# Kernel tuning notes

Measured on AMD Instinct MI355X. Metric: run time of the kernel, lower is better.

## Reference

```python
import jax, jax.numpy as jnp
import numpy as np

N_ATOM, N_QUERY, KNN = 100000, 20000, 32
E = N_QUERY * KNN
HID, EDGE_F, HEADS = 128, 16, 8
D_HEAD = HID // HEADS
LN_EPS = 1e-5


def setup_inputs() -> dict:
    key = jax.random.key(0)
    ks = jax.random.split(key, 16)
    s = 1.0 / np.sqrt(HID)
    src = jax.random.randint(ks[0], (E,), 0, N_ATOM)
    dst = jnp.repeat(jnp.arange(N_QUERY), KNN)  # each query has KNN incoming edges
    return {
        "h_atom": jax.random.normal(ks[1], (N_ATOM, HID), jnp.float32),
        "h_query": jax.random.normal(ks[2], (N_QUERY, HID), jnp.float32),
        "edge_attr": jax.random.uniform(ks[3], (E, EDGE_F), jnp.float32),
        "W_q": jax.random.normal(ks[4], (HID, HID), jnp.float32) * s,
        "W_k": jax.random.normal(ks[5], (HID, HID), jnp.float32) * s,
        "W_v": jax.random.normal(ks[6], (HID, HID), jnp.float32) * s,
        "W_rbf": jax.random.normal(ks[7], (HEADS, EDGE_F), jnp.float32) * (1.0 / np.sqrt(EDGE_F)),
        "W1": jax.random.normal(ks[8], (HID, 2 * HID), jnp.float32) * (1.0 / np.sqrt(2 * HID)),
        "b1": jnp.zeros((HID,), jnp.float32),
        "W2": jax.random.normal(ks[9], (HID, HID), jnp.float32) * s,
        "b2": jnp.zeros((HID,), jnp.float32),
        "ln_gamma": jnp.ones((HID,), jnp.float32),
        "ln_beta": jnp.zeros((HID,), jnp.float32),
        "edge_index": jnp.stack([src, dst]),
        "n_query": N_QUERY,
    }


def reference(h_atom, h_query, edge_attr, W_q, W_k, W_v, W_rbf, W1, b1, W2, b2,
              ln_gamma, ln_beta, edge_index, n_query):
    src, dst = edge_index[0], edge_index[1]
    En = src.shape[0]
    # gather + project, per-edge multi-head Q/K/V  [E, H, d]
    Q = (h_query[dst] @ W_q.T).reshape(En, HEADS, D_HEAD)
    K = (h_atom[src] @ W_k.T).reshape(En, HEADS, D_HEAD)
    V = (h_atom[src] @ W_v.T).reshape(En, HEADS, D_HEAD)
    scores = jnp.einsum("ehd,ehd->eh", Q, K) / np.sqrt(D_HEAD) + edge_attr @ W_rbf.T  # [E,H]
    # segment softmax over edges sharing the same dst query, per head
    seg_max = jax.lax.stop_gradient(jax.ops.segment_max(scores, dst, num_segments=n_query))
    ex = jnp.exp(scores - seg_max[dst])
    denom = jax.ops.segment_sum(ex, dst, num_segments=n_query)
    alpha = ex / (denom[dst] + 1e-16)  # [E,H]
    # weighted scatter-add aggregation
    msgs = (alpha[:, :, None] * V).reshape(En, HID)
    agg = jax.ops.segment_sum(msgs, dst, num_segments=n_query)  # [Nq, HID]
    # update MLP + residual + LayerNorm
    z = jnp.concatenate([h_query, agg], axis=-1)
    delta = jax.nn.relu(z @ W1.T + b1) @ W2.T + b2
    y = h_query + delta
    mu = y.mean(-1, keepdims=True)
    var = y.var(-1, keepdims=True)
    return (y - mu) / jnp.sqrt(var + LN_EPS) * ln_gamma + ln_beta
```

## Files before the change

### kernel.cpp

```cpp
#include <hip/hip_runtime.h>
#include <hip/hip_bf16.h>
#include <math.h>

#define N_ATOM   100000
#define N_QUERY  20000
#define KNN      32

typedef __attribute__((ext_vector_type(8))) short  short8;
typedef __attribute__((ext_vector_type(4))) float  floatx4;
typedef __attribute__((ext_vector_type(2))) float  fx2;

static __device__ __forceinline__ unsigned short f2bf_bits(float f) {
  union { __hip_bfloat16 h; unsigned short u; } cv;
  cv.h = __float2bfloat16(f);
  return cv.u;
}
static __device__ __forceinline__ float bflo(unsigned int u) { return __uint_as_float(u << 16); }
static __device__ __forceinline__ float bfhi(unsigned int u) { return __uint_as_float(u & 0xffff0000u); }

__global__ void pack_all_kernel(const float* __restrict__ Wq, const float* __restrict__ Wk,
                                const float* __restrict__ Wv, const float* __restrict__ W1,
                                const float* __restrict__ W2,
                                unsigned short* __restrict__ WKVp, unsigned short* __restrict__ WQp,
                                unsigned short* __restrict__ W1p,  unsigned short* __restrict__ W2p) {
  int tid = blockIdx.x * blockDim.x + threadIdx.x;
  if (tid >= 98304) return;
  const float *Wa, *Wb; int nsplit, Kd, Nd; unsigned short* dst; float scale = 1.0f;
  int t = tid;
  if (t < 32768)      { Wa = Wk; Wb = Wv; nsplit = 128; Kd = 128; Nd = 256; dst = WKVp; }
  else if (t < 49152) { t -= 32768; Wa = Wq; Wb = Wq; nsplit = 128; Kd = 128; Nd = 128; dst = WQp; scale = 0.25f; }
  else if (t < 81920) { t -= 49152; Wa = W1; Wb = W1; nsplit = 128; Kd = 256; Nd = 128; dst = W1p; }
  else                { t -= 81920; Wa = W2; Wb = W2; nsplit = 128; Kd = 128; Nd = 128; dst = W2p; }
  int j    = t & 7;
  int lane = (t >> 3) & 63;
  int t2   = t >> 9;
  int NT   = Nd >> 4;
  int ntile = t2 % NT;
  int ktile = t2 / NT;
  int k = ktile * 32 + (lane >> 4) * 8 + j;
  int n = ntile * 16 + (lane & 15);
  float v = (n < nsplit) ? Wa[(size_t)n * Kd + k] : Wb[(size_t)(n - nsplit) * Kd + k];
  dst[t] = f2bf_bits(v * scale);
}

__global__ __launch_bounds__(256) void gemm_kvq(
    const float* __restrict__ h_atom, const float* __restrict__ h_query,
    const unsigned short* __restrict__ WKVp, const unsigned short* __restrict__ WQp,
    unsigned char* __restrict__ Kp8, unsigned char* __restrict__ Vp8,
    unsigned short* __restrict__ Qb) {
  constexpr int KB = (N_ATOM + 63) / 64;
  __shared__ char lds[16384];
  const int l    = threadIdx.x & 63;
  const int w    = threadIdx.x >> 6;
  const int quad = l >> 4;
  const int col0 = l & 15;

  if ((int)blockIdx.x < KB) {
    const int row0 = blockIdx.x * 64 + w * 16;
    int arow = row0 + col0;
    if (arow >= N_ATOM) arow = N_ATOM - 1;

    const float* aptr = h_atom + (size_t)arow * 128 + quad * 8;
    floatx4 a[8];
#pragma unroll
    for (int k0 = 0; k0 < 4; k0++) {
      a[2 * k0]     = *(const floatx4*)(aptr + k0 * 32);
      a[2 * k0 + 1] = *(const floatx4*)(aptr + k0 * 32 + 4);
    }
    short8 af[4];
#pragma unroll
    for (int k0 = 0; k0 < 4; k0++) {
      af[k0][0] = (short)f2bf_bits(a[2*k0][0]); af[k0][1] = (short)f2bf_bits(a[2*k0][1]);
      af[k0][2] = (short)f2bf_bits(a[2*k0][2]); af[k0][3] = (short)f2bf_bits(a[2*k0][3]);
      af[k0][4] = (short)f2bf_bits(a[2*k0+1][0]); af[k0][5] = (short)f2bf_bits(a[2*k0+1][1]);
      af[k0][6] = (short)f2bf_bits(a[2*k0+1][2]); af[k0][7] = (short)f2bf_bits(a[2*k0+1][3]);
    }

    floatx4 acc[16];
#pragma unroll
    for (int i = 0; i < 16; i++) acc[i] = (floatx4){0.f, 0.f, 0.f, 0.f};
#pragma unroll
    for (int k0 = 0; k0 < 4; k0++) {
      const unsigned short* bbase = WKVp + (size_t)k0 * 16 * 512 + l * 8;
#pragma unroll
      for (int nt = 0; nt < 16; nt++) {
        short8 bf = *(const short8*)(bbase + nt * 512);
        acc[nt] = __builtin_amdgcn_mfma_f32_16x16x32_bf16(af[k0], bf, acc[nt], 0, 0, 0);
      }
    }
#pragma unroll
    for (int nt = 0; nt < 16; nt++) {
#pragma unroll
      for (int r = 0; r < 4; r++) {
        int rl = w * 16 + quad * 4 + r;
        int c  = nt * 16 + col0;
        int pk = __builtin_amdgcn_cvt_pk_fp8_f32(acc[nt][r], acc[nt][r], 0, false);
        if (c < 128) lds[rl * 128 + c] = (char)(pk & 0xff);
        else         lds[8192 + rl * 128 + (c - 128)] = (char)(pk & 0xff);
      }
    }
    __syncthreads();
    const int row0g = blockIdx.x * 64;
#pragma unroll
    for (int it = 0; it < 2; it++) {
      int off = threadIdx.x * 16 + it * 4096;
      if (row0g + (off >> 7) < N_ATOM)
        *(float4*)(Kp8 + (size_t)row0g * 128 + off) = *(const float4*)&lds[off];
    }
#pragma unroll
    for (int it = 0; it < 2; it++) {
      int off = threadIdx.x * 16 + it * 4096;
      if (row0g + (off >> 7) < N_ATOM)
        *(float4*)(Vp8 + (size_t)row0g * 128 + off) = *(const float4*)&lds[8192 + off];
    }
  } else {
    const int row0 = ((int)blockIdx.x - KB) * 64 + w * 16;
    int arow = row0 + col0;
    if (arow >= N_QUERY) arow = N_QUERY - 1;
    floatx4 acc[8];
#pragma unroll
    for (int i = 0; i < 8; i++) acc[i] = (floatx4){0.f, 0.f, 0.f, 0.f};
    const float* aptr = h_query + (size_t)arow * 128 + quad * 8;
#pragma unroll
    for (int k0 = 0; k0 < 128; k0 += 32) {
      floatx4 a0 = *(const floatx4*)(aptr + k0);
      floatx4 a1 = *(const floatx4*)(aptr + k0 + 4);
      short8 af;
      af[0] = (short)f2bf_bits(a0[0]); af[1] = (short)f2bf_bits(a0[1]);
      af[2] = (short)f2bf_bits(a0[2]); af[3] = (short)f2bf_bits(a0[3]);
      af[4] = (short)f2bf_bits(a1[0]); af[5] = (short)f2bf_bits(a1[1]);
      af[6] = (short)f2bf_bits(a1[2]); af[7] = (short)f2bf_bits(a1[3]);
      const unsigned short* bbase = WQp + (size_t)(k0 >> 5) * 8 * 512 + l * 8;
#pragma unroll
      for (int nt = 0; nt < 8; nt++) {
        short8 bf = *(const short8*)(bbase + nt * 512);
        acc[nt] = __builtin_amdgcn_mfma_f32_16x16x32_bf16(af, bf, acc[nt], 0, 0, 0);
      }
    }
#pragma unroll
    for (int nt = 0; nt < 8; nt++) {
#pragma unroll
      for (int r = 0; r < 4; r++) {
        int row = row0 + quad * 4 + r;
        if (row < N_QUERY) Qb[(size_t)row * 128 + nt * 16 + col0] = f2bf_bits(acc[nt][r]);
      }
    }
  }
}

__global__ __launch_bounds__(256) void attn_kernel(
    const unsigned short* __restrict__ Qb,
    const unsigned char* __restrict__ Kp8,
    const unsigned char* __restrict__ Vp8,
    const float* __restrict__ edge_attr,
    const float* __restrict__ Wrbf,
    const int* __restrict__ src,
    float* __restrict__ Agg) {
  const int l = threadIdx.x & 63;
  const int w = threadIdx.x >> 6;
  const int q = blockIdx.x * 4 + w;
  const int j = l >> 3;
  const int h = l & 7;

  const int e0 = q * KNN;
  int srcj = (l < KNN) ? src[e0 + l] : 0;

  float qd[16];
  {
    const unsigned int* qp = (const unsigned int*)(Qb + (size_t)q * 128 + h * 16);
#pragma unroll
    for (int i = 0; i < 8; i++) {
      unsigned int u = qp[i];
      qd[2 * i] = bflo(u); qd[2 * i + 1] = bfhi(u);
    }
  }
  float wr[16];
  {
    const float* wp = Wrbf + h * 16;
#pragma unroll
    for (int i = 0; i < 16; i++) wr[i] = wp[i];
  }

  float acc[16];
#pragma unroll
  for (int i = 0; i < 16; i++) acc[i] = 0.f;
  float lsum = 0.f;

#pragma unroll
  for (int p = 0; p < 4; p++) {
    const int e = p * 8 + j;
    int s = __shfl(srcj, e, 64);
    uint4 kq = *(const uint4*)(Kp8 + (size_t)s * 128 + h * 16);
    uint4 vq = *(const uint4*)(Vp8 + (size_t)s * 128 + h * 16);
    const float4* ep = (const float4*)(edge_attr + (size_t)(e0 + e) * 16);
    float4 ea0 = ep[0], ea1 = ep[1], ea2 = ep[2], ea3 = ep[3];

    float kd = 0.f;
    {
      fx2 f0, f1;
      f0 = __builtin_amdgcn_cvt_pk_f32_fp8((int)kq.x, false);
      f1 = __builtin_amdgcn_cvt_pk_f32_fp8((int)kq.x, true);
      kd += qd[0] * f0[0] + qd[1] * f0[1] + qd[2] * f1[0] + qd[3] * f1[1];
      f0 = __builtin_amdgcn_cvt_pk_f32_fp8((int)kq.y, false);
      f1 = __builtin_amdgcn_cvt_pk_f32_fp8((int)kq.y, true);
      kd += qd[4] * f0[0] + qd[5] * f0[1] + qd[6] * f1[0] + qd[7] * f1[1];
      f0 = __builtin_amdgcn_cvt_pk_f32_fp8((int)kq.z, false);
      f1 = __builtin_amdgcn_cvt_pk_f32_fp8((int)kq.z, true);
      kd += qd[8] * f0[0] + qd[9] * f0[1] + qd[10] * f1[0] + qd[11] * f1[1];
      f0 = __builtin_amdgcn_cvt_pk_f32_fp8((int)kq.w, false);
      f1 = __builtin_amdgcn_cvt_pk_f32_fp8((int)kq.w, true);
      kd += qd[12] * f0[0] + qd[13] * f0[1] + qd[14] * f1[0] + qd[15] * f1[1];
    }
    float ed = wr[0]*ea0.x + wr[1]*ea0.y + wr[2]*ea0.z + wr[3]*ea0.w
             + wr[4]*ea1.x + wr[5]*ea1.y + wr[6]*ea1.z + wr[7]*ea1.w
             + wr[8]*ea2.x + wr[9]*ea2.y + wr[10]*ea2.z + wr[11]*ea2.w
             + wr[12]*ea3.x + wr[13]*ea3.y + wr[14]*ea3.z + wr[15]*ea3.w;

    float pe = __expf(kd + ed);
    lsum += pe;
    {
      fx2 g0, g1;
      g0 = __builtin_amdgcn_cvt_pk_f32_fp8((int)vq.x, false);
      g1 = __builtin_amdgcn_cvt_pk_f32_fp8((int)vq.x, true);
      acc[0] += pe * g0[0]; acc[1] += pe * g0[1]; acc[2] += pe * g1[0]; acc[3] += pe * g1[1];
      g0 = __builtin_amdgcn_cvt_pk_f32_fp8((int)vq.y, false);
      g1 = __builtin_amdgcn_cvt_pk_f32_fp8((int)vq.y, true);
      acc[4] += pe * g0[0]; acc[5] += pe * g0[1]; acc[6] += pe * g1[0]; acc[7] += pe * g1[1];
      g0 = __builtin_amdgcn_cvt_pk_f32_fp8((int)vq.z, false);
      g1 = __builtin_amdgcn_cvt_pk_f32_fp8((int)vq.z, true);
      acc[8] += pe * g0[0]; acc[9] += pe * g0[1]; acc[10] += pe * g1[0]; acc[11] += pe * g1[1];
      g0 = __builtin_amdgcn_cvt_pk_f32_fp8((int)vq.w, false);
      g1 = __builtin_amdgcn_cvt_pk_f32_fp8((int)vq.w, true);
      acc[12] += pe * g0[0]; acc[13] += pe * g0[1]; acc[14] += pe * g1[0]; acc[15] += pe * g1[1];
    }
  }

#pragma unroll
  for (int mask = 8; mask <= 32; mask <<= 1) {
    lsum += __shfl_xor(lsum, mask, 64);
#pragma unroll
    for (int i = 0; i < 16; i++) acc[i] += __shfl_xor(acc[i], mask, 64);
  }
  float inv = 1.f / (lsum + 1e-16f);
  float* dst = Agg + (size_t)q * 128 + h * 16;
  if (j == 0) {
    float4 o0 = {acc[0] * inv, acc[1] * inv, acc[2] * inv, acc[3] * inv};
    float4 o1 = {acc[4] * inv, acc[5] * inv, acc[6] * inv, acc[7] * inv};
    *(float4*)(dst)     = o0;
    *(float4*)(dst + 4) = o1;
  } else if (j == 1) {
    float4 o2 = {acc[8] * inv, acc[9] * inv, acc[10] * inv, acc[11] * inv};
    float4 o3 = {acc[12] * inv, acc[13] * inv, acc[14] * inv, acc[15] * inv};
    *(float4*)(dst + 8)  = o2;
    *(float4*)(dst + 12) = o3;
  }
}

__global__ __launch_bounds__(256) void mlp_kernel(
    const float* __restrict__ h_query, const float* __restrict__ Agg,
    const unsigned short* __restrict__ W1p, const unsigned short* __restrict__ W2p,
    const float* __restrict__ b1, const float* __restrict__ b2,
    const float* __restrict__ gamma, const float* __restrict__ beta,
    float* __restrict__ out) {
  constexpr int M = N_QUERY;
  constexpr int STRIDE = 136;
  __shared__ unsigned short hid[64 * STRIDE];

  const int l    = threadIdx.x & 63;
  const int w    = threadIdx.x >> 6;
  const int quad = l >> 4;
  const int col0 = l & 15;
  const int row0 = blockIdx.x * 64 + w * 16;
  int arow = row0 + col0;
  if (arow >= M) arow = M - 1;

  floatx4 acc[8];
#pragma unroll
  for (int i = 0; i < 8; i++) acc[i] = (floatx4){0.f, 0.f, 0.f, 0.f};
#pragma unroll
  for (int k0 = 0; k0 < 256; k0 += 32) {
    const float* sp = (k0 < 128) ? (h_query + (size_t)arow * 128 + k0)
                                 : (Agg + (size_t)arow * 128 + (k0 - 128));
    floatx4 a0 = *(const floatx4*)(sp + quad * 8);
    floatx4 a1 = *(const floatx4*)(sp + quad * 8 + 4);
    short8 af;
    af[0] = (short)f2bf_bits(a0[0]); af[1] = (short)f2bf_bits(a0[1]);
    af[2] = (short)f2bf_bits(a0[2]); af[3] = (short)f2bf_bits(a0[3]);
    af[4] = (short)f2bf_bits(a1[0]); af[5] = (short)f2bf_bits(a1[1]);
    af[6] = (short)f2bf_bits(a1[2]); af[7] = (short)f2bf_bits(a1[3]);
    const unsigned short* bbase = W1p + (size_t)(k0 >> 5) * 8 * 512 + l * 8;
#pragma unroll
    for (int nt = 0; nt < 8; nt++) {
      short8 bf = *(const short8*)(bbase + nt * 512);
      acc[nt] = __builtin_amdgcn_mfma_f32_16x16x32_bf16(af, bf, acc[nt], 0, 0, 0);
    }
  }
#pragma unroll
  for (int nt = 0; nt < 8; nt++) {
#pragma unroll
    for (int r = 0; r < 4; r++) {
      int rl = w * 16 + quad * 4 + r;
      float v = acc[nt][r] + b1[nt * 16 + col0];
      hid[rl * STRIDE + nt * 16 + col0] = f2bf_bits(fmaxf(v, 0.f));
    }
  }
  __syncthreads();

  floatx4 acc2[8];
#pragma unroll
  for (int i = 0; i < 8; i++) acc2[i] = (floatx4){0.f, 0.f, 0.f, 0.f};
  const int rloc = w * 16 + col0;
#pragma unroll
  for (int k0 = 0; k0 < 128; k0 += 32) {
    short8 af = *(const short8*)(hid + rloc * STRIDE + k0 + quad * 8);
    const unsigned short* bbase = W2p + (size_t)(k0 >> 5) * 8 * 512 + l * 8;
#pragma unroll
    for (int nt = 0; nt < 8; nt++) {
      short8 bf = *(const short8*)(bbase + nt * 512);
      acc2[nt] = __builtin_amdgcn_mfma_f32_16x16x32_bf16(af, bf, acc2[nt], 0, 0, 0);
    }
  }

#pragma unroll
  for (int r = 0; r < 4; r++) {
    int row = row0 + quad * 4 + r;
    int rr  = row < M ? row : M - 1;
    float v[8];
    float s1 = 0.f, s2 = 0.f;
#pragma unroll
    for (int nt = 0; nt < 8; nt++) {
      int c = nt * 16 + col0;
      v[nt] = acc2[nt][r] + b2[c] + h_query[(size_t)rr * 128 + c];
      s1 += v[nt];
    }
    s1 += __shfl_xor(s1, 1, 64); s1 += __shfl_xor(s1, 2, 64);
    s1 += __shfl_xor(s1, 4, 64); s1 += __shfl_xor(s1, 8, 64);
#pragma unroll
    for (int nt = 0; nt < 8; nt++) s2 += v[nt] * v[nt];
    s2 += __shfl_xor(s2, 1, 64); s2 += __shfl_xor(s2, 2, 64);
    s2 += __shfl_xor(s2, 4, 64); s2 += __shfl_xor(s2, 8, 64);
    float mean = s1 * (1.0f / 128.0f);
    float var  = s2 * (1.0f / 128.0f) - mean * mean;
    float rstd = rsqrtf(var + 1e-5f);
    if (row < M) {
#pragma unroll
      for (int nt = 0; nt < 8; nt++) {
        int c = nt * 16 + col0;
        out[(size_t)row * 128 + c] = (v[nt] - mean) * rstd * gamma[c] + beta[c];
      }
    }
  }
}

extern "C" void kernel_launch(void* const* d_in, const int* in_sizes, int n_in,
                              void* d_out, int out_size, void* d_ws, size_t ws_size,
                              hipStream_t stream) {
  const float* h_atom    = (const float*)d_in[0];
  const float* h_query   = (const float*)d_in[1];
  const float* edge_attr = (const float*)d_in[2];
  const float* W_q  = (const float*)d_in[3];
  const float* W_k  = (const float*)d_in[4];
  const float* W_v  = (const float*)d_in[5];
  const float* Wrbf = (const float*)d_in[6];
  const float* W1   = (const float*)d_in[7];
  const float* b1   = (const float*)d_in[8];
  const float* W2   = (const float*)d_in[9];
  const float* b2   = (const float*)d_in[10];
  const float* ln_g = (const float*)d_in[11];
  const float* ln_b = (const float*)d_in[12];
  const int* edge_index = (const int*)d_in[13];
  float* out = (float*)d_out;

  char* ws = (char*)d_ws;
  unsigned char*  Kp8 = (unsigned char*)(ws);
  unsigned char*  Vp8 = (unsigned char*)(ws + 12800000);
  unsigned short* Qb  = (unsigned short*)(ws + 25600000);
  float* Agg          = (float*)(ws + 30720000);
  unsigned short* WKVp = (unsigned short*)(ws + 40960000);
  unsigned short* WQp  = WKVp + 32768;
  unsigned short* W1p  = WQp  + 16384;
  unsigned short* W2p  = W1p  + 32768;

  pack_all_kernel<<<(98304 + 255) / 256, 256, 0, stream>>>(
      W_q, W_k, W_v, W1, W2, WKVp, WQp, W1p, W2p);

  constexpr int KB = (N_ATOM + 63) / 64;
  constexpr int QB = (N_QUERY + 63) / 64;
  gemm_kvq<<<KB + QB, 256, 0, stream>>>(h_atom, h_query, WKVp, WQp, Kp8, Vp8, Qb);

  attn_kernel<<<N_QUERY / 4, 256, 0, stream>>>(Qb, Kp8, Vp8, edge_attr, Wrbf, edge_index, Agg);

  mlp_kernel<<<(N_QUERY + 63) / 64, 256, 0, stream>>>(
      h_query, Agg, W1p, W2p, b1, b2, ln_g, ln_b, out);
}
```

Baseline: 220.1 us.

## Transpose MFMA operands for vector stores, hoist attention loads, use split-reduce

Swaps the A/B operands of every MFMA so each lane holds four consecutive output columns of one row. This lets the K/V/Q, hidden and output epilogues use packed 4-byte, 8-byte and float4 stores, with a padded LDS stride to reduce bank conflicts. The attention kernel issues all gather loads (K, V, edge_attr, Q) up front to raise memory-level parallelism, and replaces the full butterfly reduction with a halving split-reduce that ends with a float2 store per lane. It also adds a launch-bounds occupancy hint, which may raise register pressure given the many live loads.

```diff
diff --git a/kernel.cpp b/kernel.cpp
--- a/kernel.cpp
+++ b/kernel.cpp
@@ -49,7 +49,8 @@
     unsigned char* __restrict__ Kp8, unsigned char* __restrict__ Vp8,
     unsigned short* __restrict__ Qb) {
   constexpr int KB = (N_ATOM + 63) / 64;
-  __shared__ char lds[16384];
+  constexpr int LSTR = 160;
+  __shared__ char lds[2 * 64 * LSTR];
   const int l    = threadIdx.x & 63;
   const int w    = threadIdx.x >> 6;
   const int quad = l >> 4;
@@ -85,33 +86,35 @@
 #pragma unroll
       for (int nt = 0; nt < 16; nt++) {
         short8 bf = *(const short8*)(bbase + nt * 512);
-        acc[nt] = __builtin_amdgcn_mfma_f32_16x16x32_bf16(af[k0], bf, acc[nt], 0, 0, 0);
+        acc[nt] = __builtin_amdgcn_mfma_f32_16x16x32_bf16(bf, af[k0], acc[nt], 0, 0, 0);
       }
     }
-#pragma unroll
-    for (int nt = 0; nt < 16; nt++) {
-#pragma unroll
-      for (int r = 0; r < 4; r++) {
-        int rl = w * 16 + quad * 4 + r;
-        int c  = nt * 16 + col0;
-        int pk = __builtin_amdgcn_cvt_pk_fp8_f32(acc[nt][r], acc[nt][r], 0, false);
-        if (c < 128) lds[rl * 128 + c] = (char)(pk & 0xff);
-        else         lds[8192 + rl * 128 + (c - 128)] = (char)(pk & 0xff);
+    {
+      const int rl = w * 16 + col0;
+#pragma unroll
+      for (int nt = 0; nt < 16; nt++) {
+        int pk = __builtin_amdgcn_cvt_pk_fp8_f32(acc[nt][0], acc[nt][1], 0, false);
+        pk     = __builtin_amdgcn_cvt_pk_fp8_f32(acc[nt][2], acc[nt][3], pk, true);
+        const int c = nt * 16 + quad * 4;
+        if (c < 128) *(int*)&lds[rl * LSTR + c] = pk;
+        else         *(int*)&lds[64 * LSTR + rl * LSTR + (c - 128)] = pk;
       }
     }
     __syncthreads();
     const int row0g = blockIdx.x * 64;
 #pragma unroll
     for (int it = 0; it < 2; it++) {
-      int off = threadIdx.x * 16 + it * 4096;
-      if (row0g + (off >> 7) < N_ATOM)
-        *(float4*)(Kp8 + (size_t)row0g * 128 + off) = *(const float4*)&lds[off];
+      int linear = threadIdx.x * 16 + it * 4096;
+      int row = linear >> 7, col = linear & 127;
+      if (row0g + row < N_ATOM)
+        *(float4*)(Kp8 + (size_t)(row0g + row) * 128 + col) = *(const float4*)&lds[row * LSTR + col];
     }
 #pragma unroll
     for (int it = 0; it < 2; it++) {
-      int off = threadIdx.x * 16 + it * 4096;
-      if (row0g + (off >> 7) < N_ATOM)
-        *(float4*)(Vp8 + (size_t)row0g * 128 + off) = *(const float4*)&lds[8192 + off];
+      int linear = threadIdx.x * 16 + it * 4096;
+      int row = linear >> 7, col = linear & 127;
+      if (row0g + row < N_ATOM)
+        *(float4*)(Vp8 + (size_t)(row0g + row) * 128 + col) = *(const float4*)&lds[64 * LSTR + row * LSTR + col];
     }
   } else {
     const int row0 = ((int)blockIdx.x - KB) * 64 + w * 16;
@@ -134,21 +137,23 @@
 #pragma unroll
       for (int nt = 0; nt < 8; nt++) {
         short8 bf = *(const short8*)(bbase + nt * 512);
-        acc[nt] = __builtin_amdgcn_mfma_f32_16x16x32_bf16(af, bf, acc[nt], 0, 0, 0);
+        acc[nt] = __builtin_amdgcn_mfma_f32_16x16x32_bf16(bf, af, acc[nt], 0, 0, 0);
       }
     }
-#pragma unroll
-    for (int nt = 0; nt < 8; nt++) {
-#pragma unroll
-      for (int r = 0; r < 4; r++) {
-        int row = row0 + quad * 4 + r;
-        if (row < N_QUERY) Qb[(size_t)row * 128 + nt * 16 + col0] = f2bf_bits(acc[nt][r]);
+    const int row = row0 + col0;
+    if (row < N_QUERY) {
+#pragma unroll
+      for (int nt = 0; nt < 8; nt++) {
+        unsigned u0 = (unsigned)f2bf_bits(acc[nt][0]) | ((unsigned)f2bf_bits(acc[nt][1]) << 16);
+        unsigned u1 = (unsigned)f2bf_bits(acc[nt][2]) | ((unsigned)f2bf_bits(acc[nt][3]) << 16);
+        uint2 uu; uu.x = u0; uu.y = u1;
+        *(uint2*)(Qb + (size_t)row * 128 + nt * 16 + quad * 4) = uu;
       }
     }
   }
 }
 
-__global__ __launch_bounds__(256) void attn_kernel(
+__global__ __launch_bounds__(256, 4) void attn_kernel(
     const unsigned short* __restrict__ Qb,
     const unsigned char* __restrict__ Kp8,
     const unsigned char* __restrict__ Vp8,
@@ -161,40 +166,70 @@
   const int q = blockIdx.x * 4 + w;
   const int j = l >> 3;
   const int h = l & 7;
-
   const int e0 = q * KNN;
+
   int srcj = (l < KNN) ? src[e0 + l] : 0;
 
+  const float4* ep0 = (const float4*)(edge_attr + (size_t)(e0 +  0 + j) * 16);
+  const float4* ep1 = (const float4*)(edge_attr + (size_t)(e0 +  8 + j) * 16);
+  const float4* ep2 = (const float4*)(edge_attr + (size_t)(e0 + 16 + j) * 16);
+  const float4* ep3 = (const float4*)(edge_attr + (size_t)(e0 + 24 + j) * 16);
+  float4 a0 = ep0[0], a1 = ep0[1], a2 = ep0[2], a3 = ep0[3];
+  float4 b0 = ep1[0], b1 = ep1[1], b2 = ep1[2], b3 = ep1[3];
+
+  const uint4* qp = (const uint4*)(Qb + (size_t)q * 128 + h * 16);
+  uint4 qA = qp[0], qB = qp[1];
+  const float4* wp = (const float4*)(Wrbf + h * 16);
+  float4 w0 = wp[0], w1 = wp[1], w2 = wp[2], w3 = wp[3];
+
+  int s0 = __shfl(srcj,      j, 64);
+  int s1 = __shfl(srcj,  8 + j, 64);
+  int s2 = __shfl(srcj, 16 + j, 64);
+  int s3 = __shfl(srcj, 24 + j, 64);
+
+  uint4 kq0 = *(const uint4*)(Kp8 + (size_t)s0 * 128 + h * 16);
+  uint4 kq1 = *(const uint4*)(Kp8 + (size_t)s1 * 128 + h * 16);
+  uint4 kq2 = *(const uint4*)(Kp8 + (size_t)s2 * 128 + h * 16);
+  uint4 kq3 = *(const uint4*)(Kp8 + (size_t)s3 * 128 + h * 16);
+  uint4 vq0 = *(const uint4*)(Vp8 + (size_t)s0 * 128 + h * 16);
+  uint4 vq1 = *(const uint4*)(Vp8 + (size_t)s1 * 128 + h * 16);
+  uint4 vq2 = *(const uint4*)(Vp8 + (size_t)s2 * 128 + h * 16);
+  uint4 vq3 = *(const uint4*)(Vp8 + (size_t)s3 * 128 + h * 16);
+
+  float4 c0 = ep2[0], c1 = ep2[1], c2 = ep2[2], c3 = ep2[3];
+
+  float ed0 = w0.x*a0.x + w0.y*a0.y + w0.z*a0.z + w0.w*a0.w
+            + w1.x*a1.x + w1.y*a1.y + w1.z*a1.z + w1.w*a1.w
+            + w2.x*a2.x + w2.y*a2.y + w2.z*a2.z + w2.w*a2.w
+            + w3.x*a3.x + w3.y*a3.y + w3.z*a3.z + w3.w*a3.w;
+
+  float4 d0 = ep3[0], d1 = ep3[1], d2 = ep3[2], d3 = ep3[3];
+
+  float ed1 = w0.x*b0.x + w0.y*b0.y + w0.z*b0.z + w0.w*b0.w
+            + w1.x*b1.x + w1.y*b1.y + w1.z*b1.z + w1.w*b1.w
+            + w2.x*b2.x + w2.y*b2.y + w2.z*b2.z + w2.w*b2.w
+            + w3.x*b3.x + w3.y*b3.y + w3.z*b3.z + w3.w*b3.w;
+  float ed2 = w0.x*c0.x + w0.y*c0.y + w0.z*c0.z + w0.w*c0.w
+            + w1.x*c1.x + w1.y*c1.y + w1.z*c1.z + w1.w*c1.w
+            + w2.x*c2.x + w2.y*c2.y + w2.z*c2.z + w2.w*c2.w
+            + w3.x*c3.x + w3.y*c3.y + w3.z*c3.z + w3.w*c3.w;
+  float ed3 = w0.x*d0.x + w0.y*d0.y + w0.z*d0.z + w0.w*d0.w
+            + w1.x*d1.x + w1.y*d1.y + w1.z*d1.z + w1.w*d1.w
+            + w2.x*d2.x + w2.y*d2.y + w2.z*d2.z + w2.w*d2.w
+            + w3.x*d3.x + w3.y*d3.y + w3.z*d3.z + w3.w*d3.w;
+
   float qd[16];
-  {
-    const unsigned int* qp = (const unsigned int*)(Qb + (size_t)q * 128 + h * 16);
-#pragma unroll
-    for (int i = 0; i < 8; i++) {
-      unsigned int u = qp[i];
-      qd[2 * i] = bflo(u); qd[2 * i + 1] = bfhi(u);
-    }
-  }
-  float wr[16];
-  {
-    const float* wp = Wrbf + h * 16;
-#pragma unroll
-    for (int i = 0; i < 16; i++) wr[i] = wp[i];
-  }
+  qd[0]  = bflo(qA.x); qd[1]  = bfhi(qA.x); qd[2]  = bflo(qA.y); qd[3]  = bfhi(qA.y);
+  qd[4]  = bflo(qA.z); qd[5]  = bfhi(qA.z); qd[6]  = bflo(qA.w); qd[7]  = bfhi(qA.w);
+  qd[8]  = bflo(qB.x); qd[9]  = bfhi(qB.x); qd[10] = bflo(qB.y); qd[11] = bfhi(qB.y);
+  qd[12] = bflo(qB.z); qd[13] = bfhi(qB.z); qd[14] = bflo(qB.w); qd[15] = bfhi(qB.w);
 
   float acc[16];
 #pragma unroll
   for (int i = 0; i < 16; i++) acc[i] = 0.f;
   float lsum = 0.f;
 
-#pragma unroll
-  for (int p = 0; p < 4; p++) {
-    const int e = p * 8 + j;
-    int s = __shfl(srcj, e, 64);
-    uint4 kq = *(const uint4*)(Kp8 + (size_t)s * 128 + h * 16);
-    uint4 vq = *(const uint4*)(Vp8 + (size_t)s * 128 + h * 16);
-    const float4* ep = (const float4*)(edge_attr + (size_t)(e0 + e) * 16);
-    float4 ea0 = ep[0], ea1 = ep[1], ea2 = ep[2], ea3 = ep[3];
-
+  auto dopass = [&](const uint4& kq, const uint4& vq, float ed) {
     float kd = 0.f;
     {
       fx2 f0, f1;
@@ -211,11 +246,6 @@
       f1 = __builtin_amdgcn_cvt_pk_f32_fp8((int)kq.w, true);
       kd += qd[12] * f0[0] + qd[13] * f0[1] + qd[14] * f1[0] + qd[15] * f1[1];
     }
-    float ed = wr[0]*ea0.x + wr[1]*ea0.y + wr[2]*ea0.z + wr[3]*ea0.w
-             + wr[4]*ea1.x + wr[5]*ea1.y + wr[6]*ea1.z + wr[7]*ea1.w
-             + wr[8]*ea2.x + wr[9]*ea2.y + wr[10]*ea2.z + wr[11]*ea2.w
-             + wr[12]*ea3.x + wr[13]*ea3.y + wr[14]*ea3.z + wr[15]*ea3.w;
-
     float pe = __expf(kd + ed);
     lsum += pe;
     {
@@ -233,27 +263,43 @@
       g1 = __builtin_amdgcn_cvt_pk_f32_fp8((int)vq.w, true);
       acc[12] += pe * g0[0]; acc[13] += pe * g0[1]; acc[14] += pe * g1[0]; acc[15] += pe * g1[1];
     }
-  }
-
-#pragma unroll
-  for (int mask = 8; mask <= 32; mask <<= 1) {
-    lsum += __shfl_xor(lsum, mask, 64);
-#pragma unroll
-    for (int i = 0; i < 16; i++) acc[i] += __shfl_xor(acc[i], mask, 64);
+  };
+  dopass(kq0, vq0, ed0);
+  dopass(kq1, vq1, ed1);
+  dopass(kq2, vq2, ed2);
+  dopass(kq3, vq3, ed3);
+
+  lsum += __shfl_xor(lsum, 8, 64);
+  lsum += __shfl_xor(lsum, 16, 64);
+  lsum += __shfl_xor(lsum, 32, 64);
+
+  float r8[8];
+  const bool hiA = (l & 32) != 0;
+#pragma unroll
+  for (int i = 0; i < 8; i++) {
+    float keep = hiA ? acc[i + 8] : acc[i];
+    float send = hiA ? acc[i]     : acc[i + 8];
+    r8[i] = keep + __shfl_xor(send, 32, 64);
+  }
+  float r4[4];
+  const bool hiB = (l & 16) != 0;
+#pragma unroll
+  for (int i = 0; i < 4; i++) {
+    float keep = hiB ? r8[i + 4] : r8[i];
+    float send = hiB ? r8[i]     : r8[i + 4];
+    r4[i] = keep + __shfl_xor(send, 16, 64);
+  }
+  float r2[2];
+  const bool hiC = (l & 8) != 0;
+#pragma unroll
+  for (int i = 0; i < 2; i++) {
+    float keep = hiC ? r4[i + 1 + 1] : r4[i];
+    float send = hiC ? r4[i]         : r4[i + 2];
+    r2[i] = keep + __shfl_xor(send, 8, 64);
   }
   float inv = 1.f / (lsum + 1e-16f);
-  float* dst = Agg + (size_t)q * 128 + h * 16;
-  if (j == 0) {
-    float4 o0 = {acc[0] * inv, acc[1] * inv, acc[2] * inv, acc[3] * inv};
-    float4 o1 = {acc[4] * inv, acc[5] * inv, acc[6] * inv, acc[7] * inv};
-    *(float4*)(dst)     = o0;
-    *(float4*)(dst + 4) = o1;
-  } else if (j == 1) {
-    float4 o2 = {acc[8] * inv, acc[9] * inv, acc[10] * inv, acc[11] * inv};
-    float4 o3 = {acc[12] * inv, acc[13] * inv, acc[14] * inv, acc[15] * inv};
-    *(float4*)(dst + 8)  = o2;
-    *(float4*)(dst + 12) = o3;
-  }
+  float2 o; o.x = r2[0] * inv; o.y = r2[1] * inv;
+  *(float2*)(Agg + (size_t)q * 128 + h * 16 + 2 * j) = o;
 }
 
 __global__ __launch_bounds__(256) void mlp_kernel(
@@ -292,16 +338,21 @@
 #pragma unroll
     for (int nt = 0; nt < 8; nt++) {
       short8 bf = *(const short8*)(bbase + nt * 512);
-      acc[nt] = __builtin_amdgcn_mfma_f32_16x16x32_bf16(af, bf, acc[nt], 0, 0, 0);
-    }
-  }
-#pragma unroll
-  for (int nt = 0; nt < 8; nt++) {
-#pragma unroll
-    for (int r = 0; r < 4; r++) {
-      int rl = w * 16 + quad * 4 + r;
-      float v = acc[nt][r] + b1[nt * 16 + col0];
-      hid[rl * STRIDE + nt * 16 + col0] = f2bf_bits(fmaxf(v, 0.f));
+      acc[nt] = __builtin_amdgcn_mfma_f32_16x16x32_bf16(bf, af, acc[nt], 0, 0, 0);
+    }
+  }
+  {
+    const int rl = w * 16 + col0;
+#pragma unroll
+    for (int nt = 0; nt < 8; nt++) {
+      const int c = nt * 16 + quad * 4;
+      float4 bb = *(const float4*)(b1 + c);
+      unsigned u0 = (unsigned)f2bf_bits(fmaxf(acc[nt][0] + bb.x, 0.f))
+                  | ((unsigned)f2bf_bits(fmaxf(acc[nt][1] + bb.y, 0.f)) << 16);
+      unsigned u1 = (unsigned)f2bf_bits(fmaxf(acc[nt][2] + bb.z, 0.f))
+                  | ((unsigned)f2bf_bits(fmaxf(acc[nt][3] + bb.w, 0.f)) << 16);
+      uint2 uu; uu.x = u0; uu.y = u1;
+      *(uint2*)(hid + rl * STRIDE + c) = uu;
     }
   }
   __syncthreads();
@@ -317,37 +368,44 @@
 #pragma unroll
     for (int nt = 0; nt < 8; nt++) {
       short8 bf = *(const short8*)(bbase + nt * 512);
-      acc2[nt] = __builtin_amdgcn_mfma_f32_16x16x32_bf16(af, bf, acc2[nt], 0, 0, 0);
-    }
-  }
-
-#pragma unroll
-  for (int r = 0; r < 4; r++) {
-    int row = row0 + quad * 4 + r;
-    int rr  = row < M ? row : M - 1;
-    float v[8];
-    float s1 = 0.f, s2 = 0.f;
+      acc2[nt] = __builtin_amdgcn_mfma_f32_16x16x32_bf16(bf, af, acc2[nt], 0, 0, 0);
+    }
+  }
+
+  const int rowq = row0 + col0;
+  const int rr   = rowq < M ? rowq : M - 1;
+  float v[8][4];
+  float s1 = 0.f, s2 = 0.f;
+#pragma unroll
+  for (int nt = 0; nt < 8; nt++) {
+    const int c = nt * 16 + quad * 4;
+    float4 hq = *(const float4*)(h_query + (size_t)rr * 128 + c);
+    float4 bb = *(const float4*)(b2 + c);
+    float t0 = acc2[nt][0] + bb.x + hq.x;
+    float t1 = acc2[nt][1] + bb.y + hq.y;
+    float t2 = acc2[nt][2] + bb.z + hq.z;
+    float t3 = acc2[nt][3] + bb.w + hq.w;
+    v[nt][0] = t0; v[nt][1] = t1; v[nt][2] = t2; v[nt][3] = t3;
+    s1 += t0 + t1 + t2 + t3;
+    s2 += t0 * t0 + t1 * t1 + t2 * t2 + t3 * t3;
+  }
+  s1 += __shfl_xor(s1, 16, 64); s1 += __shfl_xor(s1, 32, 64);
+  s2 += __shfl_xor(s2, 16, 64); s2 += __shfl_xor(s2, 32, 64);
+  float mean = s1 * (1.0f / 128.0f);
+  float var  = s2 * (1.0f / 128.0f) - mean * mean;
+  float rstd = rsqrtf(var + 1e-5f);
+  if (rowq < M) {
 #pragma unroll
     for (int nt = 0; nt < 8; nt++) {
-      int c = nt * 16 + col0;
-      v[nt] = acc2[nt][r] + b2[c] + h_query[(size_t)rr * 128 + c];
-      s1 += v[nt];
-    }
-    s1 += __shfl_xor(s1, 1, 64); s1 += __shfl_xor(s1, 2, 64);
-    s1 += __shfl_xor(s1, 4, 64); s1 += __shfl_xor(s1, 8, 64);
-#pragma unroll
-    for (int nt = 0; nt < 8; nt++) s2 += v[nt] * v[nt];
-    s2 += __shfl_xor(s2, 1, 64); s2 += __shfl_xor(s2, 2, 64);
-    s2 += __shfl_xor(s2, 4, 64); s2 += __shfl_xor(s2, 8, 64);
-    float mean = s1 * (1.0f / 128.0f);
-    float var  = s2 * (1.0f / 128.0f) - mean * mean;
-    float rstd = rsqrtf(var + 1e-5f);
-    if (row < M) {
-#pragma unroll
-      for (int nt = 0; nt < 8; nt++) {
-        int c = nt * 16 + col0;
-        out[(size_t)row * 128 + c] = (v[nt] - mean) * rstd * gamma[c] + beta[c];
-      }
+      const int c = nt * 16 + quad * 4;
+      float4 gg = *(const float4*)(gamma + c);
+      float4 be = *(const float4*)(beta + c);
+      float4 o;
+      o.x = (v[nt][0] - mean) * rstd * gg.x + be.x;
+      o.y = (v[nt][1] - mean) * rstd * gg.y + be.y;
+      o.z = (v[nt][2] - mean) * rstd * gg.z + be.z;
+      o.w = (v[nt][3] - mean) * rstd * gg.w + be.w;
+      *(float4*)(out + (size_t)rowq * 128 + c) = o;
     }
   }
 }
```

Measured after the change: 214.5 us. 2.6% less time.
